# Optimization experiments

Hardware: AMD Instinct MI355X
Metric: run time of the kernel (lower is better)

The kernel has to match this reference:

```python
import jax, jax.numpy as jnp
import numpy as np
import math

N_NODES = 100000
N_PAIRS = 640000
F_TOTAL = 128
N_HEADS = 8
HEAD_DIM = F_TOTAL // N_HEADS  # 16


def setup_inputs() -> dict:
    key = jax.random.key(0)
    ks = jax.random.split(key, 8)
    x = jax.random.normal(ks[0], (N_NODES, F_TOTAL), dtype=jnp.float32)
    w_ij = jax.random.normal(ks[1], (N_PAIRS, F_TOTAL), dtype=jnp.float32)
    idx_i = jax.random.randint(ks[2], (N_PAIRS,), 0, N_NODES, dtype=jnp.int32)
    idx_j = jax.random.randint(ks[3], (N_PAIRS,), 0, N_NODES, dtype=jnp.int32)
    phi_r_cut = jax.random.uniform(ks[4], (N_PAIRS,), dtype=jnp.float32)
    # per-head linear weights, nn.Linear convention: y = x @ W.T, W: (out, in)
    s = 1.0 / math.sqrt(HEAD_DIM)
    wq = jax.random.uniform(ks[5], (N_HEADS, HEAD_DIM, HEAD_DIM), jnp.float32, -s, s)
    wk = jax.random.uniform(ks[6], (N_HEADS, HEAD_DIM, HEAD_DIM), jnp.float32, -s, s)
    wv = jax.random.uniform(ks[7], (N_HEADS, HEAD_DIM, HEAD_DIM), jnp.float32, -s, s)
    return {"x": x, "w_ij": w_ij, "idx_i": idx_i, "idx_j": idx_j,
            "phi_r_cut": phi_r_cut, "wq": wq, "wk": wk, "wv": wv}


def reference(x, w_ij, idx_i, idx_j, phi_r_cut, wq, wk, wv):
    n, f = x.shape
    h, d = wq.shape[0], wq.shape[1]
    # split into heads: (H, n, d) and (H, P, d)
    xh = x.reshape(n, h, d).transpose(1, 0, 2)
    wh = w_ij.reshape(-1, h, d).transpose(1, 0, 2)
    # per-head linear projections (y = x @ W.T)
    q = jnp.einsum('hnd,hed->hne', xh, wq)  # (H, n, d)
    k = jnp.einsum('hnd,hed->hne', xh, wk)
    v = jnp.einsum('hnd,hed->hne', xh, wv)
    # filter-modulated dot-product attention coefficients per pair
    alpha = (q[:, idx_i] * wh * k[:, idx_j]).sum(-1) / math.sqrt(d)  # (H, P)
    alpha = alpha * phi_r_cut[None, :]
    # message + scatter-add aggregation
    msg = alpha[..., None] * v[:, idx_j]  # (H, P, d)
    y = jax.vmap(lambda m: jax.ops.segment_sum(m, idx_i, num_segments=n))(msg)  # (H, n, d)
    return y.transpose(1, 0, 2).reshape(n, f)
```

## Files before the change

### kernel.cpp

```cpp
#include <hip/hip_runtime.h>

#define F_TOTAL 128
#define N_HEADS 8
#define HEAD_DIM 16
#define SCAN_ITEMS 1024

typedef float vf4 __attribute__((ext_vector_type(4)));
typedef int   vi4 __attribute__((ext_vector_type(4)));
typedef float vf2 __attribute__((ext_vector_type(2)));

__global__ __launch_bounds__(256) void proj_hist_kernel(
    const float* __restrict__ x,
    const float* __restrict__ wq,
    const float* __restrict__ wk,
    const float* __restrict__ wv,
    const int*   __restrict__ idx_i,
    float* __restrict__ q, float* __restrict__ kv,
    int*   __restrict__ hist,
    int n_nodes, int n_pairs)
{
    const int gid = blockIdx.x * 256 + threadIdx.x;
    const int stride = gridDim.x * 256;
    const int f = gid & (F_TOTAL - 1);

    float rq[16], rk[16], rv[16];
    const float4* wq4 = (const float4*)wq;
    const float4* wk4 = (const float4*)wk;
    const float4* wv4 = (const float4*)wv;
    #pragma unroll
    for (int d4 = 0; d4 < 4; ++d4) {
        float4 a = wq4[f * 4 + d4];
        rq[d4*4+0]=a.x; rq[d4*4+1]=a.y; rq[d4*4+2]=a.z; rq[d4*4+3]=a.w;
        float4 b = wk4[f * 4 + d4];
        rk[d4*4+0]=b.x; rk[d4*4+1]=b.y; rk[d4*4+2]=b.z; rk[d4*4+3]=b.w;
        float4 c = wv4[f * 4 + d4];
        rv[d4*4+0]=c.x; rv[d4*4+1]=c.y; rv[d4*4+2]=c.z; rv[d4*4+3]=c.w;
    }
    const int lanebase = (f & 112) & 63;

    const int total = n_nodes * F_TOTAL;
    for (int idx = gid; idx < total; idx += stride) {
        const float xval = __builtin_nontemporal_load(x + idx);
        float aq = 0.f, ak = 0.f, av = 0.f;
        #pragma unroll
        for (int d = 0; d < 16; ++d) {
            const float xv = __shfl(xval, lanebase + d);
            aq += xv * rq[d];
            ak += xv * rk[d];
            av += xv * rv[d];
        }
        q[idx] = aq;
        ((vf2*)kv)[idx] = (vf2){ak, av};
    }

    for (int p = gid; p < n_pairs; p += stride)
        atomicAdd(&hist[idx_i[p]], 1);
}

__global__ __launch_bounds__(256) void scan_reduce_kernel(
    const int* __restrict__ hist, int* __restrict__ blockSums, int n)
{
    __shared__ int ls[256];
    const int t = threadIdx.x;
    const int base = blockIdx.x * SCAN_ITEMS + t * 4;
    int s = 0;
    if (base + 3 < n) {
        int4 h = *(const int4*)(hist + base);
        s = h.x + h.y + h.z + h.w;
    } else {
        for (int kk = 0; kk < 4; ++kk)
            if (base + kk < n) s += hist[base + kk];
    }
    ls[t] = s;
    __syncthreads();
    for (int off = 128; off > 0; off >>= 1) {
        if (t < off) ls[t] += ls[t + off];
        __syncthreads();
    }
    if (t == 0) blockSums[blockIdx.x] = ls[0];
}

__global__ __launch_bounds__(128) void scan_spine_kernel(
    int* __restrict__ blockSums, int nblk)
{
    __shared__ int ls[128];
    const int t = threadIdx.x;
    const int val = (t < nblk) ? blockSums[t] : 0;
    ls[t] = val;
    __syncthreads();
    for (int off = 1; off < 128; off <<= 1) {
        int add = (t >= off) ? ls[t - off] : 0;
        __syncthreads();
        ls[t] += add;
        __syncthreads();
    }
    if (t < nblk) blockSums[t] = ls[t] - val;
}

__global__ __launch_bounds__(256) void scan_apply_kernel(
    const int* __restrict__ hist, const int* __restrict__ blockSums,
    int* __restrict__ offsets, int n)
{
    __shared__ int ls[256];
    const int t = threadIdx.x;
    const int base = blockIdx.x * SCAN_ITEMS + t * 4;
    int h0 = 0, h1 = 0, h2 = 0, h3 = 0;
    if (base + 3 < n) {
        int4 h = *(const int4*)(hist + base);
        h0 = h.x; h1 = h.y; h2 = h.z; h3 = h.w;
    } else {
        if (base + 0 < n) h0 = hist[base + 0];
        if (base + 1 < n) h1 = hist[base + 1];
        if (base + 2 < n) h2 = hist[base + 2];
        if (base + 3 < n) h3 = hist[base + 3];
    }
    const int tsum = h0 + h1 + h2 + h3;
    ls[t] = tsum;
    __syncthreads();
    for (int off = 1; off < 256; off <<= 1) {
        int add = (t >= off) ? ls[t - off] : 0;
        __syncthreads();
        ls[t] += add;
        __syncthreads();
    }
    int off = blockSums[blockIdx.x] + (ls[t] - tsum);
    if (base + 0 < n) offsets[base + 0] = off; off += h0;
    if (base + 1 < n) offsets[base + 1] = off; off += h1;
    if (base + 2 < n) offsets[base + 2] = off; off += h2;
    if (base + 3 < n) offsets[base + 3] = off;
}

__global__ __launch_bounds__(256) void scatter_kernel(
    const int* __restrict__ idx_i, const int* __restrict__ idx_j,
    const float* __restrict__ phi,
    int* __restrict__ offsets,
    vi4* __restrict__ meta,
    int n_pairs)
{
    const int p = blockIdx.x * 256 + threadIdx.x;
    if (p < n_pairs) {
        const int i = idx_i[p];
        const int pos = atomicAdd(&offsets[i], 1);
        meta[pos] = (vi4){p, idx_j[p], __float_as_int(phi[p]), 0};
    }
}

__global__ __launch_bounds__(256) void segment_kernel(
    const float* __restrict__ q,
    const float* __restrict__ kv,
    const float* __restrict__ w_ij,
    const int* __restrict__ hist,
    const int* __restrict__ offsets,
    const vi4* __restrict__ meta,
    float* __restrict__ out,
    int n_nodes)
{
    const int node = blockIdx.x * 8 + (threadIdx.x >> 5);
    const int t = threadIdx.x & 31;
    if (node >= n_nodes) return;

    const int cnt = hist[node];
    const int start = offsets[node] - cnt;

    const vf4 q4 = *((const vf4*)(q + (size_t)node * F_TOTAL) + t);
    vf4 acc = (vf4){0.f, 0.f, 0.f, 0.f};

    int c = 0;
    for (; c + 2 <= cnt; c += 2) {
        const vi4 m0 = meta[start + c];
        const vi4 m1 = meta[start + c + 1];
        const vf4 w0 = __builtin_nontemporal_load(
            (const vf4*)(w_ij + (size_t)m0.x * F_TOTAL) + t);
        const vf4 w1 = __builtin_nontemporal_load(
            (const vf4*)(w_ij + (size_t)m1.x * F_TOTAL) + t);
        const vf4* kp0 = (const vf4*)(kv + (size_t)m0.y * F_TOTAL * 2) + t * 2;
        const vf4* kp1 = (const vf4*)(kv + (size_t)m1.y * F_TOTAL * 2) + t * 2;
        const vf4 a0 = kp0[0], b0 = kp0[1];
        const vf4 a1 = kp1[0], b1 = kp1[1];

        float t0 = q4.x*w0.x*a0.x + q4.y*w0.y*a0.z + q4.z*w0.z*b0.x + q4.w*w0.w*b0.z;
        float t1 = q4.x*w1.x*a1.x + q4.y*w1.y*a1.z + q4.z*w1.z*b1.x + q4.w*w1.w*b1.z;
        t0 += __shfl_xor(t0, 1); t0 += __shfl_xor(t0, 2);
        t1 += __shfl_xor(t1, 1); t1 += __shfl_xor(t1, 2);
        const float al0 = t0 * 0.25f * __int_as_float(m0.z);
        const float al1 = t1 * 0.25f * __int_as_float(m1.z);
        acc.x += al0 * a0.y; acc.y += al0 * a0.w;
        acc.z += al0 * b0.y; acc.w += al0 * b0.w;
        acc.x += al1 * a1.y; acc.y += al1 * a1.w;
        acc.z += al1 * b1.y; acc.w += al1 * b1.w;
    }
    for (; c < cnt; ++c) {
        const vi4 m0 = meta[start + c];
        const vf4 w0 = __builtin_nontemporal_load(
            (const vf4*)(w_ij + (size_t)m0.x * F_TOTAL) + t);
        const vf4* kp0 = (const vf4*)(kv + (size_t)m0.y * F_TOTAL * 2) + t * 2;
        const vf4 a0 = kp0[0], b0 = kp0[1];
        float t0 = q4.x*w0.x*a0.x + q4.y*w0.y*a0.z + q4.z*w0.z*b0.x + q4.w*w0.w*b0.z;
        t0 += __shfl_xor(t0, 1); t0 += __shfl_xor(t0, 2);
        const float al0 = t0 * 0.25f * __int_as_float(m0.z);
        acc.x += al0 * a0.y; acc.y += al0 * a0.w;
        acc.z += al0 * b0.y; acc.w += al0 * b0.w;
    }
    __builtin_nontemporal_store(acc, (vf4*)(out + (size_t)node * F_TOTAL) + t);
}

extern "C" void kernel_launch(void* const* d_in, const int* in_sizes, int n_in,
                              void* d_out, int out_size, void* d_ws, size_t ws_size,
                              hipStream_t stream)
{
    const float* x     = (const float*)d_in[0];
    const float* w_ij  = (const float*)d_in[1];
    const int*   idx_i = (const int*)d_in[2];
    const int*   idx_j = (const int*)d_in[3];
    const float* phi   = (const float*)d_in[4];
    const float* wq    = (const float*)d_in[5];
    const float* wk    = (const float*)d_in[6];
    const float* wv    = (const float*)d_in[7];

    const int n_nodes = in_sizes[0] / F_TOTAL;
    const int n_pairs = in_sizes[2];
    const size_t node_elems = (size_t)n_nodes * F_TOTAL;

    float* q         = (float*)d_ws;
    float* kv        = q + node_elems;
    vi4*   meta      = (vi4*)(kv + 2 * node_elems);
    int*   hist      = (int*)(meta + n_pairs);
    int*   offsets   = hist + n_nodes;
    int*   blockSums = offsets + n_nodes;

    hipMemsetAsync(hist, 0, (size_t)n_nodes * sizeof(int), stream);

    proj_hist_kernel<<<3072, 256, 0, stream>>>(
        x, wq, wk, wv, idx_i, q, kv, hist, n_nodes, n_pairs);

    const int nblk = (n_nodes + SCAN_ITEMS - 1) / SCAN_ITEMS;
    scan_reduce_kernel<<<nblk, 256, 0, stream>>>(hist, blockSums, n_nodes);
    scan_spine_kernel<<<1, 128, 0, stream>>>(blockSums, nblk);
    scan_apply_kernel<<<nblk, 256, 0, stream>>>(hist, blockSums, offsets, n_nodes);

    const int pair_blocks = (n_pairs + 255) / 256;
    scatter_kernel<<<pair_blocks, 256, 0, stream>>>(
        idx_i, idx_j, phi, offsets, meta, n_pairs);

    segment_kernel<<<(n_nodes + 7) / 8, 256, 0, stream>>>(
        q, kv, w_ij, hist, offsets, meta, (float*)d_out, n_nodes);
}
```

Before: 632.4 us.

## Split each node's pairs across two half-wavefronts with meta prefetch

The segment kernel now gives each node a full 64-lane wavefront instead of 32 lanes. Each half processes alternating pairs and the halves are combined with a cross-half shuffle before the store. Meta records are prefetched one iteration ahead, and meta gets padding so reads past the end stay in bounds. This adds memory-level parallelism per node to hide gather latency, at the cost of half as many nodes per block and idle lanes on low-degree nodes.

```diff
diff --git a/kernel.cpp b/kernel.cpp
--- a/kernel.cpp
+++ b/kernel.cpp
@@ -155,53 +155,68 @@
     float* __restrict__ out,
     int n_nodes)
 {
-    const int node = blockIdx.x * 8 + (threadIdx.x >> 5);
-    const int t = threadIdx.x & 31;
+    const int node = blockIdx.x * 4 + (threadIdx.x >> 6);
     if (node >= n_nodes) return;
-
-    const int cnt = hist[node];
+    const int lane = threadIdx.x & 63;
+    const int half = lane >> 5;
+    const int t    = lane & 31;
+
+    const int cnt   = hist[node];
     const int start = offsets[node] - cnt;
-
     const vf4 q4 = *((const vf4*)(q + (size_t)node * F_TOTAL) + t);
+
     vf4 acc = (vf4){0.f, 0.f, 0.f, 0.f};
 
-    int c = 0;
-    for (; c + 2 <= cnt; c += 2) {
-        const vi4 m0 = meta[start + c];
-        const vi4 m1 = meta[start + c + 1];
-        const vf4 w0 = __builtin_nontemporal_load(
-            (const vf4*)(w_ij + (size_t)m0.x * F_TOTAL) + t);
-        const vf4 w1 = __builtin_nontemporal_load(
-            (const vf4*)(w_ij + (size_t)m1.x * F_TOTAL) + t);
-        const vf4* kp0 = (const vf4*)(kv + (size_t)m0.y * F_TOTAL * 2) + t * 2;
-        const vf4* kp1 = (const vf4*)(kv + (size_t)m1.y * F_TOTAL * 2) + t * 2;
-        const vf4 a0 = kp0[0], b0 = kp0[1];
-        const vf4 a1 = kp1[0], b1 = kp1[1];
-
-        float t0 = q4.x*w0.x*a0.x + q4.y*w0.y*a0.z + q4.z*w0.z*b0.x + q4.w*w0.w*b0.z;
-        float t1 = q4.x*w1.x*a1.x + q4.y*w1.y*a1.z + q4.z*w1.z*b1.x + q4.w*w1.w*b1.z;
-        t0 += __shfl_xor(t0, 1); t0 += __shfl_xor(t0, 2);
-        t1 += __shfl_xor(t1, 1); t1 += __shfl_xor(t1, 2);
-        const float al0 = t0 * 0.25f * __int_as_float(m0.z);
-        const float al1 = t1 * 0.25f * __int_as_float(m1.z);
-        acc.x += al0 * a0.y; acc.y += al0 * a0.w;
-        acc.z += al0 * b0.y; acc.w += al0 * b0.w;
-        acc.x += al1 * a1.y; acc.y += al1 * a1.w;
-        acc.z += al1 * b1.y; acc.w += al1 * b1.w;
-    }
-    for (; c < cnt; ++c) {
-        const vi4 m0 = meta[start + c];
-        const vf4 w0 = __builtin_nontemporal_load(
-            (const vf4*)(w_ij + (size_t)m0.x * F_TOTAL) + t);
-        const vf4* kp0 = (const vf4*)(kv + (size_t)m0.y * F_TOTAL * 2) + t * 2;
-        const vf4 a0 = kp0[0], b0 = kp0[1];
-        float t0 = q4.x*w0.x*a0.x + q4.y*w0.y*a0.z + q4.z*w0.z*b0.x + q4.w*w0.w*b0.z;
-        t0 += __shfl_xor(t0, 1); t0 += __shfl_xor(t0, 2);
-        const float al0 = t0 * 0.25f * __int_as_float(m0.z);
-        acc.x += al0 * a0.y; acc.y += al0 * a0.w;
-        acc.z += al0 * b0.y; acc.w += al0 * b0.w;
-    }
-    __builtin_nontemporal_store(acc, (vf4*)(out + (size_t)node * F_TOTAL) + t);
+    const int my0 = start + half;
+    const int rem = (cnt > half) ? ((cnt - half + 1) >> 1) : 0;
+
+    if (rem > 0) {
+        vi4 m0 = meta[my0];
+        vi4 m1 = meta[my0 + 2];
+        int r = 0;
+        for (; r + 2 <= rem; r += 2) {
+            const vi4 n0 = meta[my0 + 2 * (r + 2)];
+            const vi4 n1 = meta[my0 + 2 * (r + 3)];
+            const vf4 wA = __builtin_nontemporal_load(
+                (const vf4*)(w_ij + (size_t)m0.x * F_TOTAL) + t);
+            const vf4* kpA = (const vf4*)(kv + (size_t)m0.y * F_TOTAL * 2) + t * 2;
+            const vf4 aA = kpA[0], bA = kpA[1];
+            const vf4 wB = __builtin_nontemporal_load(
+                (const vf4*)(w_ij + (size_t)m1.x * F_TOTAL) + t);
+            const vf4* kpB = (const vf4*)(kv + (size_t)m1.y * F_TOTAL * 2) + t * 2;
+            const vf4 aB = kpB[0], bB = kpB[1];
+
+            float sA = q4.x*wA.x*aA.x + q4.y*wA.y*aA.z + q4.z*wA.z*bA.x + q4.w*wA.w*bA.z;
+            float sB = q4.x*wB.x*aB.x + q4.y*wB.y*aB.z + q4.z*wB.z*bB.x + q4.w*wB.w*bB.z;
+            sA += __shfl_xor(sA, 1); sA += __shfl_xor(sA, 2);
+            sB += __shfl_xor(sB, 1); sB += __shfl_xor(sB, 2);
+            const float alA = sA * 0.25f * __int_as_float(m0.z);
+            const float alB = sB * 0.25f * __int_as_float(m1.z);
+            acc.x += alA * aA.y; acc.y += alA * aA.w;
+            acc.z += alA * bA.y; acc.w += alA * bA.w;
+            acc.x += alB * aB.y; acc.y += alB * aB.w;
+            acc.z += alB * bB.y; acc.w += alB * bB.w;
+            m0 = n0; m1 = n1;
+        }
+        if (r < rem) {
+            const vf4 wA = __builtin_nontemporal_load(
+                (const vf4*)(w_ij + (size_t)m0.x * F_TOTAL) + t);
+            const vf4* kpA = (const vf4*)(kv + (size_t)m0.y * F_TOTAL * 2) + t * 2;
+            const vf4 aA = kpA[0], bA = kpA[1];
+            float sA = q4.x*wA.x*aA.x + q4.y*wA.y*aA.z + q4.z*wA.z*bA.x + q4.w*wA.w*bA.z;
+            sA += __shfl_xor(sA, 1); sA += __shfl_xor(sA, 2);
+            const float alA = sA * 0.25f * __int_as_float(m0.z);
+            acc.x += alA * aA.y; acc.y += alA * aA.w;
+            acc.z += alA * bA.y; acc.w += alA * bA.w;
+        }
+    }
+
+    acc.x += __shfl_xor(acc.x, 32);
+    acc.y += __shfl_xor(acc.y, 32);
+    acc.z += __shfl_xor(acc.z, 32);
+    acc.w += __shfl_xor(acc.w, 32);
+    if (half == 0)
+        __builtin_nontemporal_store(acc, (vf4*)(out + (size_t)node * F_TOTAL) + t);
 }
 
 extern "C" void kernel_launch(void* const* d_in, const int* in_sizes, int n_in,
@@ -224,7 +239,7 @@
     float* q         = (float*)d_ws;
     float* kv        = q + node_elems;
     vi4*   meta      = (vi4*)(kv + 2 * node_elems);
-    int*   hist      = (int*)(meta + n_pairs);
+    int*   hist      = (int*)(meta + n_pairs + 8);
     int*   offsets   = hist + n_nodes;
     int*   blockSums = offsets + n_nodes;
 
@@ -242,6 +257,6 @@
     scatter_kernel<<<pair_blocks, 256, 0, stream>>>(
         idx_i, idx_j, phi, offsets, meta, n_pairs);
 
-    segment_kernel<<<(n_nodes + 7) / 8, 256, 0, stream>>>(
+    segment_kernel<<<(n_nodes + 3) / 4, 256, 0, stream>>>(
         q, kv, w_ij, hist, offsets, meta, (float*)d_out, n_nodes);
 }
```

New measurement: 631.4 us. No clear change (-0.1%).
